# Kernel optimization log

Measured on AMD Instinct MI355X. Metric: run time of the kernel, lower is better.

Reference implementation:

```python
import jax, jax.numpy as jnp
import numpy as np

MODEL_DIM = 1024
NUM_HEADS = 16
DEPTH = MODEL_DIM // NUM_HEADS


def setup_inputs() -> dict:
    key = jax.random.key(0)
    ks = jax.random.split(key, 9)
    B, S, D = 4, 2048, MODEL_DIM
    scale = 1.0 / np.sqrt(D)
    x = jax.random.normal(ks[0], (B, S, D), dtype=jnp.float32)
    wq = jax.random.normal(ks[1], (D, D), dtype=jnp.float32) * scale
    bq = jnp.zeros((D,), dtype=jnp.float32)
    wk = jax.random.normal(ks[2], (D, D), dtype=jnp.float32) * scale
    bk = jnp.zeros((D,), dtype=jnp.float32)
    wv = jax.random.normal(ks[3], (D, D), dtype=jnp.float32) * scale
    bv = jnp.zeros((D,), dtype=jnp.float32)
    wo = jax.random.normal(ks[4], (D, D), dtype=jnp.float32) * scale
    bo = jnp.zeros((D,), dtype=jnp.float32)
    return {"x": x, "wq": wq, "bq": bq, "wk": wk, "bk": bk,
            "wv": wv, "bv": bv, "wo": wo, "bo": bo}


def reference(x, wq, bq, wk, bk, wv, bv, wo, bo):
    B, S, D = x.shape
    H, dh = NUM_HEADS, DEPTH
    # projections
    q = (x @ wq + bq).reshape(B, S, H, dh).transpose(0, 2, 1, 3)  # [B,H,S,dh]
    k = (x @ wk + bk).reshape(B, S, H, dh).transpose(0, 2, 1, 3)
    v = (x @ wv + bv).reshape(B, S, H, dh).transpose(0, 2, 1, 3)
    # scaled dot-product attention (full score matrix, as in source)
    logits = jnp.einsum('bhqd,bhkd->bhqk', q, k) / jnp.sqrt(jnp.float32(dh))
    attn = jax.nn.softmax(logits, axis=-1)
    out = jnp.einsum('bhqk,bhkd->bhqd', attn, v)  # [B,H,S,dh]
    out = out.transpose(0, 2, 1, 3).reshape(B, S, D)
    return out @ wo + bo
```

## Files before the change

kernel.cpp:

```cpp
#include <hip/hip_runtime.h>
#include <hip/hip_bf16.h>


#define S_LEN 2048
#define DMODEL 1024
#define NH 16
#define DH 64
#define BATCH 4
#define MROWS (BATCH * S_LEN)
#define NELEM_X (MROWS * DMODEL)
#define NELEM_W (DMODEL * DMODEL)
#define NELEM_B DMODEL

typedef short short8 __attribute__((ext_vector_type(8)));
typedef float floatx4 __attribute__((ext_vector_type(4)));
typedef float floatx16 __attribute__((ext_vector_type(16)));

__device__ __forceinline__ float bf2f(unsigned short u) {
    union { unsigned int i; float f; } c; c.i = ((unsigned int)u) << 16; return c.f;
}
__device__ __forceinline__ unsigned int f2bf_pk(float lo, float hi) {
    unsigned int r;
    asm("v_cvt_pk_bf16_f32 %0, %1, %2" : "=v"(r) : "v"(lo), "v"(hi));
    return r;
}
__device__ __forceinline__ void async_copy16(const void* g, void* l) {
    __builtin_amdgcn_global_load_lds(
        (const __attribute__((address_space(1))) unsigned int*)g,
        (__attribute__((address_space(3))) unsigned int*)l, 16, 0, 0);
}

__device__ __forceinline__ floatx16 mfma32_k16(short8 a, short8 b, floatx16 c) {
    return __builtin_amdgcn_mfma_f32_32x32x16_bf16(a, b, c, 0, 0, 0);
}

__global__ void sniff_kernel(const unsigned short* __restrict__ x, int* flag) {
    __shared__ int cnt;
    if (threadIdx.x == 0) cnt = 0;
    __syncthreads();
    int c = 0;
    for (int i = threadIdx.x; i < 65536; i += 256) {
        unsigned int e = (x[i] >> 7) & 0xFFu;
        if (e >= 0xC0u) c++;
    }
    atomicAdd(&cnt, c);
    __syncthreads();
    if (threadIdx.x == 0) *flag = (cnt > 64) ? 1 : 0;
}

struct ConvArgs { const void* s[5]; unsigned short* d[5]; int n8[5]; };
__global__ void convert_all(ConvArgs a, const int* __restrict__ flag) {
    const int seg = blockIdx.y;
    const int f = *flag;
    const int n8 = a.n8[seg];
    unsigned short* dst = a.d[seg];
    int i = blockIdx.x * blockDim.x + threadIdx.x;
    const int stride = gridDim.x * blockDim.x;
    if (f) {
        const float4* s4 = (const float4*)a.s[seg];
        for (; i < n8; i += stride) {
            float4 x0 = s4[2 * i], x1 = s4[2 * i + 1];
            uint4 o;
            o.x = f2bf_pk(x0.x, x0.y); o.y = f2bf_pk(x0.z, x0.w);
            o.z = f2bf_pk(x1.x, x1.y); o.w = f2bf_pk(x1.z, x1.w);
            *(uint4*)(dst + (size_t)i * 8) = o;
        }
    } else {
        const uint4* s4 = (const uint4*)a.s[seg];
        for (; i < n8; i += stride) *(uint4*)(dst + (size_t)i * 8) = s4[i];
    }
}

struct TWArgs { const void* s[4]; unsigned short* d[4]; };
__global__ void transpose_w(TWArgs a, const int* __restrict__ flag) {
    __shared__ unsigned int Lt[64 * 33];
    const int z = blockIdx.z;
    const int f = *flag;
    const int k0 = blockIdx.x * 64, n0 = blockIdx.y * 64;
    const int t = threadIdx.x;
    const int c = t & 63, rgrp = t >> 6;

    if (f) {
        const float* W = (const float*)a.s[z];
        #pragma unroll
        for (int s = 0; s < 8; s++) {
            int r0 = rgrp * 16 + 2 * s;
            float v0 = W[(size_t)(k0 + r0) * DMODEL + n0 + c];
            float v1 = W[(size_t)(k0 + r0 + 1) * DMODEL + n0 + c];
            Lt[c * 33 + rgrp * 8 + s] = f2bf_pk(v0, v1);
        }
    } else {
        const unsigned short* W = (const unsigned short*)a.s[z];
        #pragma unroll
        for (int s = 0; s < 8; s++) {
            int r0 = rgrp * 16 + 2 * s;
            unsigned int lo = W[(size_t)(k0 + r0) * DMODEL + n0 + c];
            unsigned int hi = W[(size_t)(k0 + r0 + 1) * DMODEL + n0 + c];
            Lt[c * 33 + rgrp * 8 + s] = lo | (hi << 16);
        }
    }
    __syncthreads();
    const int row = t >> 2, j = t & 3;
    unsigned int* outp = (unsigned int*)(a.d[z] + (size_t)(n0 + row) * DMODEL + k0);
    #pragma unroll
    for (int i = 0; i < 8; i++) outp[j * 8 + i] = Lt[row * 33 + j * 8 + i];
}

__global__ void transpose_v(const unsigned short* __restrict__ vws,
                            unsigned short* __restrict__ vt) {
    __shared__ unsigned int Lt[64 * 33];
    const int tok0 = blockIdx.x * 64;
    const int bh   = blockIdx.y;
    const int b    = bh >> 4;
    const int h    = bh & 15;
    const int t = threadIdx.x;
    const int c = t & 63, rgrp = t >> 6;

    const unsigned short* src = vws + (size_t)b * S_LEN * DMODEL + h * DH;
    #pragma unroll
    for (int s = 0; s < 8; s++) {
        int r0 = rgrp * 16 + 2 * s;
        unsigned int lo = src[(size_t)(tok0 + r0) * DMODEL + c];
        unsigned int hi = src[(size_t)(tok0 + r0 + 1) * DMODEL + c];
        Lt[c * 33 + rgrp * 8 + s] = lo | (hi << 16);
    }
    __syncthreads();
    const int row = t >> 2, j = t & 3;
    unsigned int* outp = (unsigned int*)(vt + (size_t)bh * DH * S_LEN
                                            + (size_t)row * S_LEN + tok0);
    const int p2[8] = {0, 1, 4, 5, 2, 3, 6, 7};
    #pragma unroll
    for (int i = 0; i < 8; i++) outp[j * 8 + i] = Lt[row * 33 + j * 8 + p2[i]];
}

__global__ __launch_bounds__(256, 2)
void gemm_bias_kernel(const unsigned short* __restrict__ X,
                      const unsigned short* __restrict__ T0, const unsigned short* __restrict__ B0, void* __restrict__ Y0,
                      const unsigned short* __restrict__ T1, const unsigned short* __restrict__ B1, void* __restrict__ Y1,
                      const unsigned short* __restrict__ T2, const unsigned short* __restrict__ B2, void* __restrict__ Y2,
                      float os0, float os1, float os2,
                      const int* __restrict__ flag, int fp32_out)
{
    const unsigned short* Wt = T0; const unsigned short* Bi = B0; void* Y = Y0;
    float os = os0;
    if (blockIdx.z == 1) { Wt = T1; Bi = B1; Y = Y1; os = os1; }
    else if (blockIdx.z == 2) { Wt = T2; Bi = B2; Y = Y2; os = os2; }
    const int f32o = fp32_out ? (*flag) : 0;

    __shared__ __align__(16) unsigned short As[128 * 32];
    __shared__ __align__(16) unsigned short Bs[128 * 32];

    const int t    = threadIdx.x;
    const int lane = t & 63;
    const int wid  = t >> 6;
    const int quad = lane >> 4;
    const int n16  = lane & 15;
    const int wm   = wid >> 1, wn = wid & 1;

    const int m0 = blockIdx.x * 128;
    const int n0 = blockIdx.y * 128;

    floatx4 acc[4][4];
    #pragma unroll
    for (int i = 0; i < 4; i++)
        #pragma unroll
        for (int j = 0; j < 4; j++) acc[i][j] = (floatx4){0.f, 0.f, 0.f, 0.f};

    const int r = t >> 2, c8 = (t & 3) * 8;

    for (int kb = 0; kb < DMODEL; kb += 32) {
        __syncthreads();
        async_copy16(X  + (size_t)(m0 + r)      * DMODEL + kb + c8, As + r * 32 + c8);
        async_copy16(X  + (size_t)(m0 + 64 + r) * DMODEL + kb + c8, As + (64 + r) * 32 + c8);
        async_copy16(Wt + (size_t)(n0 + r)      * DMODEL + kb + c8, Bs + r * 32 + c8);
        async_copy16(Wt + (size_t)(n0 + 64 + r) * DMODEL + kb + c8, Bs + (64 + r) * 32 + c8);
        __syncthreads();

        short8 af[4], bfr[4];
        #pragma unroll
        for (int mt = 0; mt < 4; mt++)
            af[mt] = *(const short8*)(As + (wm * 64 + mt * 16 + n16) * 32 + quad * 8);
        #pragma unroll
        for (int nt = 0; nt < 4; nt++)
            bfr[nt] = *(const short8*)(Bs + (wn * 64 + nt * 16 + n16) * 32 + quad * 8);
        #pragma unroll
        for (int mt = 0; mt < 4; mt++)
            #pragma unroll
            for (int nt = 0; nt < 4; nt++)
                acc[mt][nt] = __builtin_amdgcn_mfma_f32_16x16x32_bf16(af[mt], bfr[nt], acc[mt][nt], 0, 0, 0);
    }

    float bv4[4];
    #pragma unroll
    for (int nt = 0; nt < 4; nt++) bv4[nt] = bf2f(Bi[n0 + wn * 64 + nt * 16 + n16]) * os;
    #pragma unroll
    for (int mt = 0; mt < 4; mt++)
        #pragma unroll
        for (int rr = 0; rr < 4; rr++) {
            size_t row = (size_t)(m0 + wm * 64 + mt * 16 + quad * 4 + rr);
            if (f32o) {
                #pragma unroll
                for (int nt = 0; nt < 4; nt++) {
                    int col = n0 + wn * 64 + nt * 16 + n16;
                    ((float*)Y)[row * DMODEL + col] = fmaf(acc[mt][nt][rr], os, bv4[nt]);
                }
            } else {
                #pragma unroll
                for (int np = 0; np < 2; np++) {
                    float v0 = fmaf(acc[mt][2 * np    ][rr], os, bv4[2 * np]);
                    float v1 = fmaf(acc[mt][2 * np + 1][rr], os, bv4[2 * np + 1]);
                    unsigned int pk = f2bf_pk(v0, v1);
                    int col = n0 + wn * 64 + (2 * np) * 16 + n16;
                    ((unsigned short*)Y)[row * DMODEL + col]      = (unsigned short)pk;
                    ((unsigned short*)Y)[row * DMODEL + col + 16] = (unsigned short)(pk >> 16);
                }
            }
        }
}

__global__ __launch_bounds__(256, 2)
void attn_kernel(const unsigned short* Qw,
                 const unsigned short* __restrict__ Kw,
                 const unsigned short* __restrict__ VT,
                 unsigned short* Ow)
{
    __shared__ __align__(16) unsigned short Ks[64 * 64];
    __shared__ __align__(16) unsigned short Vts[64 * 64];

    const int t    = threadIdx.x;
    const int lane = t & 63;
    const int w    = t >> 6;
    const int q32  = lane & 31;
    const int hi   = lane >> 5;
    const int r7   = q32 & 7;

    const int bid  = blockIdx.x;
    const int bh   = bid & 63;
    const int qblk = bid >> 6;
    const int b    = bh >> 4;
    const int h    = bh & 15;

    const size_t baseRow = (size_t)b * S_LEN;
    const int hoff = h * DH;
    const unsigned short* VTb = VT + (size_t)bh * DH * S_LEN;

    int qrow[2];
    short8 qf[2][4];
    #pragma unroll
    for (int g = 0; g < 2; g++) {
        qrow[g] = qblk * 256 + w * 64 + g * 32 + q32;
        #pragma unroll
        for (int ds = 0; ds < 4; ds++)
            qf[g][ds] = *(const short8*)(Qw + (baseRow + qrow[g]) * DMODEL + hoff
                                            + ds * 16 + hi * 8);
    }

    const floatx16 z16 = {0.f,0.f,0.f,0.f,0.f,0.f,0.f,0.f,
                          0.f,0.f,0.f,0.f,0.f,0.f,0.f,0.f};
    floatx16 acco[2][2];
    #pragma unroll
    for (int g = 0; g < 2; g++)
        #pragma unroll
        for (int dt = 0; dt < 2; dt++) acco[g][dt] = z16;
    float ls[2] = {0.f, 0.f};

    const int srow = t >> 2;
    const int scc  = (t & 3) * 2;
    const int kswz0 = ((scc    ) ^ (srow & 7)) * 8;
    const int kswz1 = ((scc + 1) ^ (srow & 7)) * 8;
    unsigned short* KsW = Ks  + srow * 64;
    unsigned short* VsW = Vts + srow * 64;
    const unsigned short* Kp = Kw + (baseRow + srow) * DMODEL + hoff;
    const unsigned short* Vp = VTb + (size_t)srow * S_LEN;

    float4 kr0 = *(const float4*)(Kp + scc * 8);
    float4 kr1 = *(const float4*)(Kp + scc * 8 + 8);
    float4 vr0 = *(const float4*)(Vp + scc * 8);
    float4 vr1 = *(const float4*)(Vp + scc * 8 + 8);

    for (int kb = 0; kb < S_LEN; kb += 64) {
        __syncthreads();
        *(float4*)(KsW + kswz0) = kr0;
        *(float4*)(KsW + kswz1) = kr1;
        *(float4*)(VsW + kswz0) = vr0;
        *(float4*)(VsW + kswz1) = vr1;
        if (kb + 64 < S_LEN) {
            kr0 = *(const float4*)(Kp + (size_t)(kb + 64) * DMODEL + scc * 8);
            kr1 = *(const float4*)(Kp + (size_t)(kb + 64) * DMODEL + scc * 8 + 8);
            vr0 = *(const float4*)(Vp + kb + 64 + scc * 8);
            vr1 = *(const float4*)(Vp + kb + 64 + scc * 8 + 8);
        }
        __syncthreads();

        floatx16 sf[2][2];
        #pragma unroll
        for (int g = 0; g < 2; g++)
            #pragma unroll
            for (int kt = 0; kt < 2; kt++) sf[g][kt] = z16;

        __builtin_amdgcn_s_setprio(1);
        #pragma unroll
        for (int kt = 0; kt < 2; kt++) {
            const unsigned short* Kr = Ks + (kt * 32 + q32) * 64;
            #pragma unroll
            for (int ds = 0; ds < 4; ds++) {
                short8 kf = *(const short8*)(Kr + (((ds * 2 + hi) ^ r7) * 8));
                sf[0][kt] = mfma32_k16(kf, qf[0][ds], sf[0][kt]);
                sf[1][kt] = mfma32_k16(kf, qf[1][ds], sf[1][kt]);
            }
        }
        __builtin_amdgcn_s_setprio(0);

        #pragma unroll
        for (int g = 0; g < 2; g++) {
            float lsum = 0.f;
            #pragma unroll
            for (int kt = 0; kt < 2; kt++)
                #pragma unroll
                for (int i = 0; i < 16; i++) {
                    float p = __builtin_exp2f(sf[g][kt][i]);
                    sf[g][kt][i] = p;
                    lsum += p;
                }
            ls[g] += lsum;
        }

        __builtin_amdgcn_s_setprio(1);
        #pragma unroll
        for (int kt = 0; kt < 2; kt++) {
            #pragma unroll
            for (int tt = 0; tt < 2; tt++) {
                union { unsigned int u[4]; short8 s8; } pb0, pb1;
                #pragma unroll
                for (int j = 0; j < 4; j++) {
                    pb0.u[j] = f2bf_pk(sf[0][kt][8 * tt + 2 * j],
                                       sf[0][kt][8 * tt + 2 * j + 1]);
                    pb1.u[j] = f2bf_pk(sf[1][kt][8 * tt + 2 * j],
                                       sf[1][kt][8 * tt + 2 * j + 1]);
                }
                const int vchunk = ((4 * kt + 2 * tt + hi) ^ r7) * 8;
                #pragma unroll
                for (int dt = 0; dt < 2; dt++) {
                    short8 vf = *(const short8*)(Vts + (dt * 32 + q32) * 64 + vchunk);
                    acco[0][dt] = mfma32_k16(vf, pb0.s8, acco[0][dt]);
                    acco[1][dt] = mfma32_k16(vf, pb1.s8, acco[1][dt]);
                }
            }
        }
        __builtin_amdgcn_s_setprio(0);
    }

    #pragma unroll
    for (int g = 0; g < 2; g++) {
        float l = ls[g];
        l += __shfl_xor(l, 32);
        const float rinv = 1.f / l;
        #pragma unroll
        for (int dt = 0; dt < 2; dt++) {
            #pragma unroll
            for (int m = 0; m < 4; m++) {
                uint2 o;
                o.x = f2bf_pk(acco[g][dt][4 * m] * rinv, acco[g][dt][4 * m + 1] * rinv);
                o.y = f2bf_pk(acco[g][dt][4 * m + 2] * rinv, acco[g][dt][4 * m + 3] * rinv);
                *(uint2*)(Ow + (baseRow + qrow[g]) * DMODEL + hoff
                             + dt * 32 + m * 8 + hi * 4) = o;
            }
        }
    }
}

extern "C" void kernel_launch(void* const* d_in, const int* in_sizes, int n_in,
                              void* d_out, int out_size, void* d_ws, size_t ws_size,
                              hipStream_t stream)
{
    unsigned short* base = (unsigned short*)d_ws;
    int* flag = (int*)d_ws;
    unsigned short* xc  = base + 8;
    unsigned short* wqt = xc  + NELEM_X;
    unsigned short* wkt = wqt + NELEM_W;
    unsigned short* wvt = wkt + NELEM_W;
    unsigned short* wot = wvt + NELEM_W;
    unsigned short* bqc = wot + NELEM_W;
    unsigned short* bkc = bqc + NELEM_B;
    unsigned short* bvc = bkc + NELEM_B;
    unsigned short* boc = bvc + NELEM_B;
    unsigned short* qws = boc + NELEM_B;
    unsigned short* kws = qws + NELEM_X;
    unsigned short* vws = kws + NELEM_X;
    unsigned short* aws = qws;
    unsigned short* vtw = xc;

    sniff_kernel<<<1, 256, 0, stream>>>((const unsigned short*)d_in[0], flag);

    ConvArgs ca;
    const void* csrc[5] = {d_in[0], d_in[2], d_in[4], d_in[6], d_in[8]};
    unsigned short* cdst[5] = {xc, bqc, bkc, bvc, boc};
    int cn8[5] = {NELEM_X / 8, NELEM_B / 8, NELEM_B / 8, NELEM_B / 8, NELEM_B / 8};
    for (int i = 0; i < 5; i++) { ca.s[i] = csrc[i]; ca.d[i] = cdst[i]; ca.n8[i] = cn8[i]; }
    convert_all<<<dim3(256, 5), 256, 0, stream>>>(ca, flag);

    TWArgs tw;
    const void* tsrc[4] = {d_in[1], d_in[3], d_in[5], d_in[7]};
    unsigned short* tdst[4] = {wqt, wkt, wvt, wot};
    for (int i = 0; i < 4; i++) { tw.s[i] = tsrc[i]; tw.d[i] = tdst[i]; }
    transpose_w<<<dim3(16, 16, 4), 256, 0, stream>>>(tw, flag);

    const float qscale = 0.125f * 1.44269504088896340736f;
    gemm_bias_kernel<<<dim3(64, 8, 3), 256, 0, stream>>>(
        xc, wqt, bqc, qws, wkt, bkc, kws, wvt, bvc, vws,
        qscale, 1.f, 1.f, flag, 0);

    transpose_v<<<dim3(32, 64), 256, 0, stream>>>(vws, vtw);

    attn_kernel<<<dim3(512), 256, 0, stream>>>(qws, kws, vtw, aws);

    gemm_bias_kernel<<<dim3(64, 8, 1), 256, 0, stream>>>(
        aws, wot, boc, d_out, wot, boc, d_out, wot, boc, d_out,
        1.f, 1.f, 1.f, flag, 1);
}
```

Before: 369.5 us.

## Compute softmax row sums via MFMA with ones vector and interleave per-kt stages

Replaces the scalar VALU summation of exponentiated scores with an extra MFMA against a bf16 ones vector, so the denominator accumulates on the matrix unit from the same bf16 P values used in the PV product. The QK, exp and PV stages are restructured per key tile (kt), which lowers live register pressure and lets the MFMA and exp work interleave. Global load pointers are also strength-reduced to incrementing pointers. This trades VALU adds and a cross-lane shuffle for additional MFMA issue (4 more per tile). The sum now uses bf16-rounded probabilities, which matches the numerator rounding.

```diff
diff --git a/kernel.cpp b/kernel.cpp
--- a/kernel.cpp
+++ b/kernel.cpp
@@ -257,12 +257,15 @@
 
     const floatx16 z16 = {0.f,0.f,0.f,0.f,0.f,0.f,0.f,0.f,
                           0.f,0.f,0.f,0.f,0.f,0.f,0.f,0.f};
+    const short8 ones8 = {(short)0x3F80, (short)0x3F80, (short)0x3F80, (short)0x3F80,
+                          (short)0x3F80, (short)0x3F80, (short)0x3F80, (short)0x3F80};
     floatx16 acco[2][2];
     #pragma unroll
     for (int g = 0; g < 2; g++)
         #pragma unroll
         for (int dt = 0; dt < 2; dt++) acco[g][dt] = z16;
-    float ls[2] = {0.f, 0.f};
+    floatx16 accl[2];
+    accl[0] = z16; accl[1] = z16;
 
     const int srow = t >> 2;
     const int scc  = (t & 3) * 2;
@@ -270,13 +273,15 @@
     const int kswz1 = ((scc + 1) ^ (srow & 7)) * 8;
     unsigned short* KsW = Ks  + srow * 64;
     unsigned short* VsW = Vts + srow * 64;
-    const unsigned short* Kp = Kw + (baseRow + srow) * DMODEL + hoff;
-    const unsigned short* Vp = VTb + (size_t)srow * S_LEN;
-
-    float4 kr0 = *(const float4*)(Kp + scc * 8);
-    float4 kr1 = *(const float4*)(Kp + scc * 8 + 8);
-    float4 vr0 = *(const float4*)(Vp + scc * 8);
-    float4 vr1 = *(const float4*)(Vp + scc * 8 + 8);
+    const unsigned short* Kp = Kw + (baseRow + srow) * DMODEL + hoff + scc * 8;
+    const unsigned short* Vp = VTb + (size_t)srow * S_LEN + scc * 8;
+
+    float4 kr0 = *(const float4*)(Kp);
+    float4 kr1 = *(const float4*)(Kp + 8);
+    float4 vr0 = *(const float4*)(Vp);
+    float4 vr1 = *(const float4*)(Vp + 8);
+    const unsigned short* KpL = Kp + (size_t)64 * DMODEL;
+    const unsigned short* VpL = Vp + 64;
 
     for (int kb = 0; kb < S_LEN; kb += 64) {
         __syncthreads();
@@ -285,58 +290,47 @@
         *(float4*)(VsW + kswz0) = vr0;
         *(float4*)(VsW + kswz1) = vr1;
         if (kb + 64 < S_LEN) {
-            kr0 = *(const float4*)(Kp + (size_t)(kb + 64) * DMODEL + scc * 8);
-            kr1 = *(const float4*)(Kp + (size_t)(kb + 64) * DMODEL + scc * 8 + 8);
-            vr0 = *(const float4*)(Vp + kb + 64 + scc * 8);
-            vr1 = *(const float4*)(Vp + kb + 64 + scc * 8 + 8);
+            kr0 = *(const float4*)(KpL);
+            kr1 = *(const float4*)(KpL + 8);
+            vr0 = *(const float4*)(VpL);
+            vr1 = *(const float4*)(VpL + 8);
+            KpL += (size_t)64 * DMODEL;
+            VpL += 64;
         }
         __syncthreads();
 
-        floatx16 sf[2][2];
-        #pragma unroll
-        for (int g = 0; g < 2; g++)
-            #pragma unroll
-            for (int kt = 0; kt < 2; kt++) sf[g][kt] = z16;
-
-        __builtin_amdgcn_s_setprio(1);
         #pragma unroll
         for (int kt = 0; kt < 2; kt++) {
             const unsigned short* Kr = Ks + (kt * 32 + q32) * 64;
+            floatx16 s0, s1;
+            __builtin_amdgcn_s_setprio(1);
+            {
+                short8 kf = *(const short8*)(Kr + ((hi ^ r7) * 8));
+                s0 = mfma32_k16(kf, qf[0][0], z16);
+                s1 = mfma32_k16(kf, qf[1][0], z16);
+            }
             #pragma unroll
-            for (int ds = 0; ds < 4; ds++) {
+            for (int ds = 1; ds < 4; ds++) {
                 short8 kf = *(const short8*)(Kr + (((ds * 2 + hi) ^ r7) * 8));
-                sf[0][kt] = mfma32_k16(kf, qf[0][ds], sf[0][kt]);
-                sf[1][kt] = mfma32_k16(kf, qf[1][ds], sf[1][kt]);
-            }
-        }
-        __builtin_amdgcn_s_setprio(0);
-
-        #pragma unroll
-        for (int g = 0; g < 2; g++) {
-            float lsum = 0.f;
+                s0 = mfma32_k16(kf, qf[0][ds], s0);
+                s1 = mfma32_k16(kf, qf[1][ds], s1);
+            }
+            __builtin_amdgcn_s_setprio(0);
+
             #pragma unroll
-            for (int kt = 0; kt < 2; kt++)
-                #pragma unroll
-                for (int i = 0; i < 16; i++) {
-                    float p = __builtin_exp2f(sf[g][kt][i]);
-                    sf[g][kt][i] = p;
-                    lsum += p;
-                }
-            ls[g] += lsum;
-        }
-
-        __builtin_amdgcn_s_setprio(1);
-        #pragma unroll
-        for (int kt = 0; kt < 2; kt++) {
+            for (int i = 0; i < 16; i++) {
+                s0[i] = __builtin_exp2f(s0[i]);
+                s1[i] = __builtin_exp2f(s1[i]);
+            }
+
+            __builtin_amdgcn_s_setprio(1);
             #pragma unroll
             for (int tt = 0; tt < 2; tt++) {
                 union { unsigned int u[4]; short8 s8; } pb0, pb1;
                 #pragma unroll
                 for (int j = 0; j < 4; j++) {
-                    pb0.u[j] = f2bf_pk(sf[0][kt][8 * tt + 2 * j],
-                                       sf[0][kt][8 * tt + 2 * j + 1]);
-                    pb1.u[j] = f2bf_pk(sf[1][kt][8 * tt + 2 * j],
-                                       sf[1][kt][8 * tt + 2 * j + 1]);
+                    pb0.u[j] = f2bf_pk(s0[8 * tt + 2 * j], s0[8 * tt + 2 * j + 1]);
+                    pb1.u[j] = f2bf_pk(s1[8 * tt + 2 * j], s1[8 * tt + 2 * j + 1]);
                 }
                 const int vchunk = ((4 * kt + 2 * tt + hi) ^ r7) * 8;
                 #pragma unroll
@@ -345,16 +339,16 @@
                     acco[0][dt] = mfma32_k16(vf, pb0.s8, acco[0][dt]);
                     acco[1][dt] = mfma32_k16(vf, pb1.s8, acco[1][dt]);
                 }
-            }
-        }
-        __builtin_amdgcn_s_setprio(0);
+                accl[0] = mfma32_k16(ones8, pb0.s8, accl[0]);
+                accl[1] = mfma32_k16(ones8, pb1.s8, accl[1]);
+            }
+            __builtin_amdgcn_s_setprio(0);
+        }
     }
 
     #pragma unroll
     for (int g = 0; g < 2; g++) {
-        float l = ls[g];
-        l += __shfl_xor(l, 32);
-        const float rinv = 1.f / l;
+        const float rinv = 1.f / accl[g][0];
         #pragma unroll
         for (int dt = 0; dt < 2; dt++) {
             #pragma unroll
```

After: 397.6 us. +7.6%, slower.
